# Performance work log

Hardware: AMD Instinct MI355X
Metric: run time of the kernel (lower is better)

## Reference

```python
import jax, jax.numpy as jnp
import numpy as np

DIM = 768
INNER = int(DIM * 0.125)  # 96
N_TOK = 8
EPS = 1e-5


def setup_inputs() -> dict:
    key = jax.random.key(0)
    ks = jax.random.split(key, 5)
    x = jax.random.normal(ks[0], (64, DIM, 32, 32), dtype=jnp.float32)
    gamma = jnp.ones((DIM,), jnp.float32)
    beta = jnp.zeros((DIM,), jnp.float32)
    w1 = jax.random.normal(ks[1], (DIM, INNER), jnp.float32) * 0.02
    b1 = jnp.zeros((INNER,), jnp.float32)
    w2 = jax.random.normal(ks[2], (INNER, N_TOK), jnp.float32) * 0.02
    b2 = jnp.zeros((N_TOK,), jnp.float32)
    return {"x": x, "gamma": gamma, "beta": beta, "w1": w1, "b1": b1, "w2": w2, "b2": b2}


def reference(x, gamma, beta, w1, b1, w2, b2):
    B, C, H, W = x.shape
    # torch: x.transpose(1, 3).reshape(B, H*W, C)  ([B,C,H,W] -> [B,W,H,C] -> [B,HW,C])
    t = jnp.transpose(x, (0, 3, 2, 1)).reshape(B, H * W, C)
    # LayerNorm over channel dim
    mu = jnp.mean(t, axis=-1, keepdims=True)
    var = jnp.mean(jnp.square(t - mu), axis=-1, keepdims=True)
    xn = (t - mu) * jax.lax.rsqrt(var + EPS) * gamma + beta  # [B, HW, C]
    # small MLP producing per-token attention logits
    h = jax.nn.gelu(xn @ w1 + b1, approximate=False)  # [B, HW, INNER]
    attn = jax.nn.softmax(h @ w2 + b2, axis=1)        # softmax across HW -> [B, HW, N]
    # (x.unsqueeze(-1) * attn).mean(dim=1) == einsum / HW, no [B,HW,C,N] intermediate
    out = jnp.einsum('bhc,bhn->bcn', xn, attn) / (H * W)  # [B, C, N]
    return out
```

## Files before the change

kernel.cpp:

```cpp
#include <hip/hip_runtime.h>
#include <hip/hip_bf16.h>
#include <math.h>

#define BATCH 64
#define CH    768
#define NP    1024
#define NI    96
#define NT    8
#define EPSF  1e-5f

typedef __attribute__((ext_vector_type(8))) short  short8;
typedef __attribute__((ext_vector_type(4))) float  f32x4;

__device__ __forceinline__ short bfs(float f) {
    __hip_bfloat16 h = __float2bfloat16(f);
    return *reinterpret_cast<short*>(&h);
}

__global__ __launch_bounds__(64) void k_w1pack(const float* __restrict__ w1,
                                               unsigned short* __restrict__ w1f) {
    int ks = blockIdx.x / 6, nt = blockIdx.x % 6;
    int l  = threadIdx.x;
    int n  = nt * 16 + (l & 15);
    int k0 = ks * 32 + (l >> 4) * 8;
    short8 o;
#pragma unroll
    for (int j = 0; j < 8; ++j) o[j] = bfs(w1[(size_t)(k0 + j) * NI + n]);
    *(short8*)(w1f + ((size_t)blockIdx.x * 64 + l) * 8) = o;
}

__global__ __launch_bounds__(256) void k_mlpf(const float* __restrict__ x,
        const float* __restrict__ gamma, const float* __restrict__ beta,
        const unsigned short* __restrict__ w1f,
        const float* __restrict__ b1, const float* __restrict__ w2,
        const float* __restrict__ b2,
        float2* __restrict__ stats, float* __restrict__ logits)
{
    int bid = blockIdx.x;
    int b   = bid >> 3;
    int p0  = (bid & 7) << 7;
    int tid = threadIdx.x;

    __shared__ float4 ls[8][32];
    __shared__ float4 lq[8][32];
    __shared__ float2 stl[128];

    {
        int tg = tid & 31;
        int cg = tid >> 5;
        const float* xb = x + (size_t)b * CH * NP + p0 + tg * 4;
        float4 s = make_float4(0.f,0.f,0.f,0.f);
        float4 q = make_float4(0.f,0.f,0.f,0.f);
#pragma unroll 4
        for (int c = cg; c < CH; c += 8) {
            float4 v = *(const float4*)(xb + (size_t)c * NP);
            s.x += v.x; s.y += v.y; s.z += v.z; s.w += v.w;
            q.x += v.x*v.x; q.y += v.y*v.y; q.z += v.z*v.z; q.w += v.w*v.w;
        }
        ls[cg][tg] = s; lq[cg][tg] = q;
        __syncthreads();
        if (cg == 0) {
#pragma unroll
            for (int k = 1; k < 8; ++k) {
                float4 s2 = ls[k][tg], q2 = lq[k][tg];
                s.x += s2.x; s.y += s2.y; s.z += s2.z; s.w += s2.w;
                q.x += q2.x; q.y += q2.y; q.z += q2.z; q.w += q2.w;
            }
            const float inv = 1.0f / (float)CH;
            float2 r0, r1, r2, r3;
            float mu, var;
            mu = s.x*inv; var = q.x*inv - mu*mu; r0 = make_float2(mu, rsqrtf(var + EPSF));
            mu = s.y*inv; var = q.y*inv - mu*mu; r1 = make_float2(mu, rsqrtf(var + EPSF));
            mu = s.z*inv; var = q.z*inv - mu*mu; r2 = make_float2(mu, rsqrtf(var + EPSF));
            mu = s.w*inv; var = q.w*inv - mu*mu; r3 = make_float2(mu, rsqrtf(var + EPSF));
            stl[tg*4+0] = r0; stl[tg*4+1] = r1; stl[tg*4+2] = r2; stl[tg*4+3] = r3;
            float2* st = stats + (size_t)b * NP + p0 + tg * 4;
            st[0] = r0; st[1] = r1; st[2] = r2; st[3] = r3;
        }
        __syncthreads();
    }

    int wv   = tid >> 6;
    int lane = tid & 63;
    int m    = lane & 15;
    int kg   = lane >> 4;
    int mt   = p0 + wv * 32;

    float2 st0 = stl[wv * 32 + m];
    float2 st1 = stl[wv * 32 + 16 + m];
    const float* xb = x + (size_t)b * CH * NP + mt + m;

    f32x4 accA[6], accB[6];
#pragma unroll
    for (int nt = 0; nt < 6; ++nt) {
        accA[nt] = (f32x4){0.f,0.f,0.f,0.f};
        accB[nt] = (f32x4){0.f,0.f,0.f,0.f};
    }
    const short8* wfp = (const short8*)w1f;

    for (int ks = 0; ks < 24; ++ks) {
        int cb = ks * 32 + kg * 8;
        const float* xc = xb + (size_t)cb * NP;
        float xv0[8], xv1[8];
#pragma unroll
        for (int j = 0; j < 8; ++j) {
            xv0[j] = xc[(size_t)j * NP];
            xv1[j] = xc[(size_t)j * NP + 16];
        }
        float4 g0 = *(const float4*)(gamma + cb);
        float4 g1 = *(const float4*)(gamma + cb + 4);
        float4 e0 = *(const float4*)(beta  + cb);
        float4 e1 = *(const float4*)(beta  + cb + 4);
        float gm[8] = {g0.x,g0.y,g0.z,g0.w,g1.x,g1.y,g1.z,g1.w};
        float bt[8] = {e0.x,e0.y,e0.z,e0.w,e1.x,e1.y,e1.z,e1.w};
        short8 a0, a1;
#pragma unroll
        for (int j = 0; j < 8; ++j) {
            float rg0 = st0.y * gm[j];
            float rg1 = st1.y * gm[j];
            a0[j] = bfs(fmaf(xv0[j], rg0, fmaf(-st0.x, rg0, bt[j])));
            a1[j] = bfs(fmaf(xv1[j], rg1, fmaf(-st1.x, rg1, bt[j])));
        }
        const short8* wk = wfp + (size_t)ks * 6 * 64 + lane;
#pragma unroll
        for (int nt = 0; nt < 6; ++nt) {
            short8 bf = wk[nt * 64];
            accA[nt] = __builtin_amdgcn_mfma_f32_16x16x32_bf16(a0, bf, accA[nt], 0, 0, 0);
            accB[nt] = __builtin_amdgcn_mfma_f32_16x16x32_bf16(a1, bf, accB[nt], 0, 0, 0);
        }
    }

    int nlo = lane & 15;
    float4 b2a = *(const float4*)b2;
    float4 b2b = *(const float4*)(b2 + 4);
#pragma unroll
    for (int half = 0; half < 2; ++half) {
        float lg[4][8];
#pragma unroll
        for (int r = 0; r < 4; ++r)
#pragma unroll
            for (int t = 0; t < 8; ++t) lg[r][t] = 0.f;
#pragma unroll
        for (int nt = 0; nt < 6; ++nt) {
            int n = nt * 16 + nlo;
            float b1v = b1[n];
            float4 w2a = *(const float4*)(w2 + n * 8);
            float4 w2b = *(const float4*)(w2 + n * 8 + 4);
            f32x4 ac = half ? accB[nt] : accA[nt];
#pragma unroll
            for (int r = 0; r < 4; ++r) {
                float h = ac[r] + b1v;
                h = 0.5f * h * (1.0f + erff(h * 0.70710678118654752f));
                lg[r][0] += h * w2a.x; lg[r][1] += h * w2a.y;
                lg[r][2] += h * w2a.z; lg[r][3] += h * w2a.w;
                lg[r][4] += h * w2b.x; lg[r][5] += h * w2b.y;
                lg[r][6] += h * w2b.z; lg[r][7] += h * w2b.w;
            }
        }
#pragma unroll
        for (int mask = 1; mask <= 8; mask <<= 1)
#pragma unroll
            for (int r = 0; r < 4; ++r)
#pragma unroll
                for (int t = 0; t < 8; ++t)
                    lg[r][t] += __shfl_xor(lg[r][t], mask, 64);
        if (nlo == 0) {
#pragma unroll
            for (int r = 0; r < 4; ++r) {
                int pp = mt + half * 16 + kg * 4 + r;
                float* op = logits + ((size_t)b * NP + pp) * NT;
                *(float4*)op       = make_float4(lg[r][0] + b2a.x, lg[r][1] + b2a.y,
                                                 lg[r][2] + b2a.z, lg[r][3] + b2a.w);
                *(float4*)(op + 4) = make_float4(lg[r][4] + b2b.x, lg[r][5] + b2b.y,
                                                 lg[r][6] + b2b.z, lg[r][7] + b2b.w);
            }
        }
    }
}

__global__ __launch_bounds__(256) void k_g(const float* __restrict__ logits,
        const float2* __restrict__ stats,
        unsigned short* __restrict__ gbf, float* __restrict__ S2)
{
    int b = blockIdx.x;
    int tid = threadIdx.x;
    int lane = tid & 63, wv = tid >> 6;
    __shared__ float gs[NP][NT];
    __shared__ float red[4][16];

    const float* lgp = logits + (size_t)b * NP * NT;
    const float2* stb = stats + (size_t)b * NP;
    float e[4][NT];
    float2 st4[4];
#pragma unroll
    for (int k = 0; k < 4; ++k) {
        int p = tid + 256 * k;
        float4 a  = *(const float4*)(lgp + (size_t)p * NT);
        float4 bq = *(const float4*)(lgp + (size_t)p * NT + 4);
        e[k][0]=a.x; e[k][1]=a.y; e[k][2]=a.z; e[k][3]=a.w;
        e[k][4]=bq.x; e[k][5]=bq.y; e[k][6]=bq.z; e[k][7]=bq.w;
        st4[k] = stb[p];
    }
    float mx[NT];
#pragma unroll
    for (int t = 0; t < NT; ++t)
        mx[t] = fmaxf(fmaxf(e[0][t], e[1][t]), fmaxf(e[2][t], e[3][t]));
#pragma unroll
    for (int mask = 1; mask <= 32; mask <<= 1)
#pragma unroll
        for (int t = 0; t < NT; ++t)
            mx[t] = fmaxf(mx[t], __shfl_xor(mx[t], mask, 64));
    if (lane == 0) {
#pragma unroll
        for (int t = 0; t < NT; ++t) red[wv][t] = mx[t];
    }
    __syncthreads();
#pragma unroll
    for (int t = 0; t < NT; ++t)
        mx[t] = fmaxf(fmaxf(red[0][t], red[1][t]), fmaxf(red[2][t], red[3][t]));
    __syncthreads();

    float sm[NT], s2p[NT];
#pragma unroll
    for (int t = 0; t < NT; ++t) { sm[t] = 0.f; s2p[t] = 0.f; }
#pragma unroll
    for (int k = 0; k < 4; ++k) {
        float mr = st4[k].x * st4[k].y;
#pragma unroll
        for (int t = 0; t < NT; ++t) {
            e[k][t] = expf(e[k][t] - mx[t]);
            sm[t]  += e[k][t];
            s2p[t] += mr * e[k][t];
        }
    }
#pragma unroll
    for (int mask = 1; mask <= 32; mask <<= 1)
#pragma unroll
        for (int t = 0; t < NT; ++t) {
            sm[t]  += __shfl_xor(sm[t],  mask, 64);
            s2p[t] += __shfl_xor(s2p[t], mask, 64);
        }
    if (lane == 0) {
#pragma unroll
        for (int t = 0; t < NT; ++t) { red[wv][t] = sm[t]; red[wv][8 + t] = s2p[t]; }
    }
    __syncthreads();
    float inv[NT], s2f[NT];
#pragma unroll
    for (int t = 0; t < NT; ++t) {
        float s  = red[0][t] + red[1][t] + red[2][t] + red[3][t];
        float s2 = red[0][8+t] + red[1][8+t] + red[2][8+t] + red[3][8+t];
        inv[t] = 1.0f / s;
        s2f[t] = s2 * inv[t];
    }
    if (tid < NT) S2[b * NT + tid] = s2f[tid];

#pragma unroll
    for (int k = 0; k < 4; ++k)
#pragma unroll
        for (int t = 0; t < NT; ++t)
            gs[tid + 256 * k][t] = st4[k].y * e[k][t] * inv[t];
    __syncthreads();

    unsigned short* gb = gbf + (size_t)b * 2048 * 8;
#pragma unroll
    for (int ss = 0; ss < 8; ++ss) {
        int slot   = tid * 8 + ss;
        int lane_s = slot & 63;
        int ks     = slot >> 6;
        int n      = lane_s & 15;
        int k0     = ks * 32 + (lane_s >> 4) * 8;
        short8 o = (short8){0,0,0,0,0,0,0,0};
        if (n < 8) {
#pragma unroll
            for (int j = 0; j < 8; ++j) o[j] = bfs(gs[k0 + j][n]);
        }
        *(short8*)(gb + (size_t)slot * 8) = o;
    }
}

__global__ __launch_bounds__(256) void k_outg(const float* __restrict__ x,
        const unsigned short* __restrict__ gbf, const float* __restrict__ S2,
        const float* __restrict__ gamma, const float* __restrict__ beta,
        float* __restrict__ out)
{
    int b   = blockIdx.x / 12;
    int c0  = (blockIdx.x % 12) * 64;
    int tid = threadIdx.x, lane = tid & 63, wv = tid >> 6;
    int kg  = lane >> 4, m = lane & 15, n = lane & 15;
    int cw  = c0 + wv * 16;

    const float*  xr = x + ((size_t)b * CH + cw + m) * NP + kg * 8;
    const short8* gb = (const short8*)gbf + (size_t)b * 2048;

    f32x4 acc0 = (f32x4){0.f,0.f,0.f,0.f};
    f32x4 acc1 = (f32x4){0.f,0.f,0.f,0.f};
#pragma unroll 4
    for (int ks = 0; ks < 32; ks += 2) {
        float4 v0 = *(const float4*)(xr + ks * 32);
        float4 v1 = *(const float4*)(xr + ks * 32 + 4);
        float4 v2 = *(const float4*)(xr + ks * 32 + 32);
        float4 v3 = *(const float4*)(xr + ks * 32 + 36);
        short8 a0, a1;
        a0[0]=bfs(v0.x); a0[1]=bfs(v0.y); a0[2]=bfs(v0.z); a0[3]=bfs(v0.w);
        a0[4]=bfs(v1.x); a0[5]=bfs(v1.y); a0[6]=bfs(v1.z); a0[7]=bfs(v1.w);
        a1[0]=bfs(v2.x); a1[1]=bfs(v2.y); a1[2]=bfs(v2.z); a1[3]=bfs(v2.w);
        a1[4]=bfs(v3.x); a1[5]=bfs(v3.y); a1[6]=bfs(v3.z); a1[7]=bfs(v3.w);
        short8 bf0 = gb[ks * 64 + lane];
        short8 bf1 = gb[(ks + 1) * 64 + lane];
        acc0 = __builtin_amdgcn_mfma_f32_16x16x32_bf16(a0, bf0, acc0, 0, 0, 0);
        acc1 = __builtin_amdgcn_mfma_f32_16x16x32_bf16(a1, bf1, acc1, 0, 0, 0);
    }

    if (n < NT) {
        float s2v = S2[b * NT + n];
        const float sc = 1.0f / (float)NP;
#pragma unroll
        for (int r = 0; r < 4; ++r) {
            int c = cw + kg * 4 + r;
            float val = acc0[r] + acc1[r];
            out[((size_t)b * CH + c) * NT + n] = (gamma[c] * (val - s2v) + beta[c]) * sc;
        }
    }
}

extern "C" void kernel_launch(void* const* d_in, const int* in_sizes, int n_in,
                              void* d_out, int out_size, void* d_ws, size_t ws_size,
                              hipStream_t stream) {
    const float* x     = (const float*)d_in[0];
    const float* gamma = (const float*)d_in[1];
    const float* beta  = (const float*)d_in[2];
    const float* w1    = (const float*)d_in[3];
    const float* b1    = (const float*)d_in[4];
    const float* w2    = (const float*)d_in[5];
    const float* b2    = (const float*)d_in[6];
    float* out = (float*)d_out;

    char* ws = (char*)d_ws;
    float2*         stats = (float2*)(ws + 0);
    float*          lgbuf = (float*)(ws + 524288);
    unsigned short* w1f   = (unsigned short*)(ws + 2621440);
    unsigned short* gbf   = (unsigned short*)(ws + 2768896);
    float*          S2    = (float*)(ws + 4866048);

    k_w1pack<<<24 * 6,     64,  0, stream>>>(w1, w1f);
    k_mlpf  <<<BATCH * 8,  256, 0, stream>>>(x, gamma, beta, w1f, b1, w2, b2, stats, lgbuf);
    k_g     <<<BATCH,      256, 0, stream>>>(lgbuf, stats, gbf, S2);
    k_outg  <<<BATCH * 12, 256, 0, stream>>>(x, gbf, S2, gamma, beta, out);
}
```

Measured before the change: 353.8 us.

## Fold LayerNorm into W1 GEMM epilogue and fuse softmax weights into output kernel

Gamma is folded into packed W1, and the per-column sums gamma·W1 and beta·W1+b1 are precomputed. This lets the MLP kernel feed raw x into the MFMA and apply mean/rstd afterwards, so the separate statistics pass over x is gone. The softmax/g-fragment kernel is merged into the output kernel, which recomputes the per-batch softmax in each block and keeps the bf16 fragments in LDS instead of a global round trip. The costs are redundant softmax work across 12 blocks per batch, larger LDS use, and bf16 rounding of un-normalized x, which may lose precision when the mean is large.

```diff
diff --git a/kernel.cpp b/kernel.cpp
--- a/kernel.cpp
+++ b/kernel.cpp
@@ -17,77 +17,55 @@
     return *reinterpret_cast<short*>(&h);
 }
 
-__global__ __launch_bounds__(64) void k_w1pack(const float* __restrict__ w1,
-                                               unsigned short* __restrict__ w1f) {
-    int ks = blockIdx.x / 6, nt = blockIdx.x % 6;
-    int l  = threadIdx.x;
-    int n  = nt * 16 + (l & 15);
-    int k0 = ks * 32 + (l >> 4) * 8;
-    short8 o;
-#pragma unroll
-    for (int j = 0; j < 8; ++j) o[j] = bfs(w1[(size_t)(k0 + j) * NI + n]);
-    *(short8*)(w1f + ((size_t)blockIdx.x * 64 + l) * 8) = o;
+__global__ __launch_bounds__(128) void k_prep(const float* __restrict__ w1,
+        const float* __restrict__ gamma, const float* __restrict__ beta,
+        const float* __restrict__ b1,
+        unsigned short* __restrict__ w1f, float* __restrict__ c1, float* __restrict__ gw1)
+{
+    int bid = blockIdx.x;
+    if (bid < 72) {
+        int slot = bid * 128 + threadIdx.x;
+        int l    = slot & 63;
+        int blk  = slot >> 6;
+        int ks   = blk / 6, nt = blk % 6;
+        int n    = nt * 16 + (l & 15);
+        int k0   = ks * 32 + (l >> 4) * 8;
+        short8 o;
+#pragma unroll
+        for (int j = 0; j < 8; ++j)
+            o[j] = bfs(gamma[k0 + j] * w1[(size_t)(k0 + j) * NI + n]);
+        *(short8*)(w1f + (size_t)slot * 8) = o;
+    } else {
+        int n = threadIdx.x;
+        if (n < NI) {
+            float bw = 0.f, gw = 0.f;
+#pragma unroll 4
+            for (int c = 0; c < CH; ++c) {
+                float w = w1[(size_t)c * NI + n];
+                bw = fmaf(beta[c],  w, bw);
+                gw = fmaf(gamma[c], w, gw);
+            }
+            c1[n]  = bw + b1[n];
+            gw1[n] = gw;
+        }
+    }
 }
 
 __global__ __launch_bounds__(256) void k_mlpf(const float* __restrict__ x,
-        const float* __restrict__ gamma, const float* __restrict__ beta,
         const unsigned short* __restrict__ w1f,
-        const float* __restrict__ b1, const float* __restrict__ w2,
-        const float* __restrict__ b2,
+        const float* __restrict__ c1, const float* __restrict__ gw1,
+        const float* __restrict__ w2, const float* __restrict__ b2,
         float2* __restrict__ stats, float* __restrict__ logits)
 {
-    int bid = blockIdx.x;
-    int b   = bid >> 3;
-    int p0  = (bid & 7) << 7;
-    int tid = threadIdx.x;
-
-    __shared__ float4 ls[8][32];
-    __shared__ float4 lq[8][32];
-    __shared__ float2 stl[128];
-
-    {
-        int tg = tid & 31;
-        int cg = tid >> 5;
-        const float* xb = x + (size_t)b * CH * NP + p0 + tg * 4;
-        float4 s = make_float4(0.f,0.f,0.f,0.f);
-        float4 q = make_float4(0.f,0.f,0.f,0.f);
-#pragma unroll 4
-        for (int c = cg; c < CH; c += 8) {
-            float4 v = *(const float4*)(xb + (size_t)c * NP);
-            s.x += v.x; s.y += v.y; s.z += v.z; s.w += v.w;
-            q.x += v.x*v.x; q.y += v.y*v.y; q.z += v.z*v.z; q.w += v.w*v.w;
-        }
-        ls[cg][tg] = s; lq[cg][tg] = q;
-        __syncthreads();
-        if (cg == 0) {
-#pragma unroll
-            for (int k = 1; k < 8; ++k) {
-                float4 s2 = ls[k][tg], q2 = lq[k][tg];
-                s.x += s2.x; s.y += s2.y; s.z += s2.z; s.w += s2.w;
-                q.x += q2.x; q.y += q2.y; q.z += q2.z; q.w += q2.w;
-            }
-            const float inv = 1.0f / (float)CH;
-            float2 r0, r1, r2, r3;
-            float mu, var;
-            mu = s.x*inv; var = q.x*inv - mu*mu; r0 = make_float2(mu, rsqrtf(var + EPSF));
-            mu = s.y*inv; var = q.y*inv - mu*mu; r1 = make_float2(mu, rsqrtf(var + EPSF));
-            mu = s.z*inv; var = q.z*inv - mu*mu; r2 = make_float2(mu, rsqrtf(var + EPSF));
-            mu = s.w*inv; var = q.w*inv - mu*mu; r3 = make_float2(mu, rsqrtf(var + EPSF));
-            stl[tg*4+0] = r0; stl[tg*4+1] = r1; stl[tg*4+2] = r2; stl[tg*4+3] = r3;
-            float2* st = stats + (size_t)b * NP + p0 + tg * 4;
-            st[0] = r0; st[1] = r1; st[2] = r2; st[3] = r3;
-        }
-        __syncthreads();
-    }
-
-    int wv   = tid >> 6;
-    int lane = tid & 63;
+    int bid  = blockIdx.x;
+    int b    = bid >> 3;
+    int p0   = (bid & 7) << 7;
+    int wv   = threadIdx.x >> 6;
+    int lane = threadIdx.x & 63;
     int m    = lane & 15;
     int kg   = lane >> 4;
     int mt   = p0 + wv * 32;
 
-    float2 st0 = stl[wv * 32 + m];
-    float2 st1 = stl[wv * 32 + 16 + m];
     const float* xb = x + (size_t)b * CH * NP + mt + m;
 
     f32x4 accA[6], accB[6];
@@ -96,6 +74,7 @@
         accA[nt] = (f32x4){0.f,0.f,0.f,0.f};
         accB[nt] = (f32x4){0.f,0.f,0.f,0.f};
     }
+    float s0 = 0.f, q0 = 0.f, s1 = 0.f, q1 = 0.f;
     const short8* wfp = (const short8*)w1f;
 
     for (int ks = 0; ks < 24; ++ks) {
@@ -107,19 +86,13 @@
             xv0[j] = xc[(size_t)j * NP];
             xv1[j] = xc[(size_t)j * NP + 16];
         }
-        float4 g0 = *(const float4*)(gamma + cb);
-        float4 g1 = *(const float4*)(gamma + cb + 4);
-        float4 e0 = *(const float4*)(beta  + cb);
-        float4 e1 = *(const float4*)(beta  + cb + 4);
-        float gm[8] = {g0.x,g0.y,g0.z,g0.w,g1.x,g1.y,g1.z,g1.w};
-        float bt[8] = {e0.x,e0.y,e0.z,e0.w,e1.x,e1.y,e1.z,e1.w};
         short8 a0, a1;
 #pragma unroll
         for (int j = 0; j < 8; ++j) {
-            float rg0 = st0.y * gm[j];
-            float rg1 = st1.y * gm[j];
-            a0[j] = bfs(fmaf(xv0[j], rg0, fmaf(-st0.x, rg0, bt[j])));
-            a1[j] = bfs(fmaf(xv1[j], rg1, fmaf(-st1.x, rg1, bt[j])));
+            s0 += xv0[j]; q0 = fmaf(xv0[j], xv0[j], q0);
+            s1 += xv1[j]; q1 = fmaf(xv1[j], xv1[j], q1);
+            a0[j] = bfs(xv0[j]);
+            a1[j] = bfs(xv1[j]);
         }
         const short8* wk = wfp + (size_t)ks * 6 * 64 + lane;
 #pragma unroll
@@ -130,6 +103,32 @@
         }
     }
 
+    s0 += __shfl_xor(s0, 16, 64); s0 += __shfl_xor(s0, 32, 64);
+    q0 += __shfl_xor(q0, 16, 64); q0 += __shfl_xor(q0, 32, 64);
+    s1 += __shfl_xor(s1, 16, 64); s1 += __shfl_xor(s1, 32, 64);
+    q1 += __shfl_xor(q1, 16, 64); q1 += __shfl_xor(q1, 32, 64);
+    const float invC = 1.0f / (float)CH;
+    float mu0 = s0 * invC, var0 = fmaf(-mu0, mu0, q0 * invC);
+    float mu1 = s1 * invC, var1 = fmaf(-mu1, mu1, q1 * invC);
+    float rstd0 = rsqrtf(var0 + EPSF), rstd1 = rsqrtf(var1 + EPSF);
+    float mr0 = mu0 * rstd0, mr1 = mu1 * rstd1;
+
+    if (kg == 0) {
+        float2* st = stats + (size_t)b * NP + mt + m;
+        st[0]  = make_float2(mr0, rstd0);
+        st[16] = make_float2(mr1, rstd1);
+    }
+
+    float mrs0[4], rss0[4], mrs1[4], rss1[4];
+#pragma unroll
+    for (int r = 0; r < 4; ++r) {
+        int src = 4 * kg + r;
+        mrs0[r] = __shfl(mr0,   src, 64);
+        rss0[r] = __shfl(rstd0, src, 64);
+        mrs1[r] = __shfl(mr1,   src, 64);
+        rss1[r] = __shfl(rstd1, src, 64);
+    }
+
     int nlo = lane & 15;
     float4 b2a = *(const float4*)b2;
     float4 b2b = *(const float4*)(b2 + 4);
@@ -143,13 +142,16 @@
 #pragma unroll
         for (int nt = 0; nt < 6; ++nt) {
             int n = nt * 16 + nlo;
-            float b1v = b1[n];
+            float c1v  = c1[n];
+            float gw1v = gw1[n];
             float4 w2a = *(const float4*)(w2 + n * 8);
             float4 w2b = *(const float4*)(w2 + n * 8 + 4);
             f32x4 ac = half ? accB[nt] : accA[nt];
 #pragma unroll
             for (int r = 0; r < 4; ++r) {
-                float h = ac[r] + b1v;
+                float rs = half ? rss1[r] : rss0[r];
+                float mr = half ? mrs1[r] : mrs0[r];
+                float h = fmaf(rs, ac[r], fmaf(-mr, gw1v, c1v));
                 h = 0.5f * h * (1.0f + erff(h * 0.70710678118654752f));
                 lg[r][0] += h * w2a.x; lg[r][1] += h * w2a.y;
                 lg[r][2] += h * w2a.z; lg[r][3] += h * w2a.w;
@@ -178,15 +180,19 @@
     }
 }
 
-__global__ __launch_bounds__(256) void k_g(const float* __restrict__ logits,
-        const float2* __restrict__ stats,
-        unsigned short* __restrict__ gbf, float* __restrict__ S2)
+__global__ __launch_bounds__(256) void k_outg(const float* __restrict__ x,
+        const float* __restrict__ logits, const float2* __restrict__ stats,
+        const float* __restrict__ gamma, const float* __restrict__ beta,
+        float* __restrict__ out)
 {
-    int b = blockIdx.x;
+    int b   = blockIdx.x / 12;
+    int c0  = (blockIdx.x % 12) * 64;
     int tid = threadIdx.x;
     int lane = tid & 63, wv = tid >> 6;
-    __shared__ float gs[NP][NT];
+
+    __shared__ unsigned short gfrag[2048 * 8];
     __shared__ float red[4][16];
+    __shared__ float s2s[NT];
 
     const float* lgp = logits + (size_t)b * NP * NT;
     const float2* stb = stats + (size_t)b * NP;
@@ -225,12 +231,11 @@
     for (int t = 0; t < NT; ++t) { sm[t] = 0.f; s2p[t] = 0.f; }
 #pragma unroll
     for (int k = 0; k < 4; ++k) {
-        float mr = st4[k].x * st4[k].y;
 #pragma unroll
         for (int t = 0; t < NT; ++t) {
             e[k][t] = expf(e[k][t] - mx[t]);
             sm[t]  += e[k][t];
-            s2p[t] += mr * e[k][t];
+            s2p[t] = fmaf(st4[k].x, e[k][t], s2p[t]);
         }
     }
 #pragma unroll
@@ -242,56 +247,43 @@
         }
     if (lane == 0) {
 #pragma unroll
-        for (int t = 0; t < NT; ++t) { red[wv][t] = sm[t]; red[wv][8 + t] = s2p[t]; }
-    }
-    __syncthreads();
-    float inv[NT], s2f[NT];
-#pragma unroll
-    for (int t = 0; t < NT; ++t) {
-        float s  = red[0][t] + red[1][t] + red[2][t] + red[3][t];
-        float s2 = red[0][8+t] + red[1][8+t] + red[2][8+t] + red[3][8+t];
-        inv[t] = 1.0f / s;
-        s2f[t] = s2 * inv[t];
-    }
-    if (tid < NT) S2[b * NT + tid] = s2f[tid];
-
-#pragma unroll
-    for (int k = 0; k < 4; ++k)
+        for (int t = 0; t < NT; ++t) { red[wv][t] = sm[t]; }
+    }
+    __syncthreads();
+    float inv[NT];
+#pragma unroll
+    for (int t = 0; t < NT; ++t)
+        inv[t] = 1.0f / (red[0][t] + red[1][t] + red[2][t] + red[3][t]);
+    __syncthreads();
+    if (lane == 0) {
+#pragma unroll
+        for (int t = 0; t < NT; ++t) red[wv][t] = s2p[t];
+    }
+    __syncthreads();
+    if (tid < NT)
+        s2s[tid] = (red[0][tid] + red[1][tid] + red[2][tid] + red[3][tid]) * inv[tid];
+
+#pragma unroll
+    for (int q = 0; q < 4; ++q) {
+        int idx  = tid * 4 + q;
+        int slot = (idx >> 3) * 16 + 8 + (idx & 7);
+        *(short8*)(gfrag + (size_t)slot * 8) = (short8){0,0,0,0,0,0,0,0};
+    }
+#pragma unroll
+    for (int k = 0; k < 4; ++k) {
+        int p = tid + 256 * k;
+        int base = ((p >> 5) * 64 + ((p >> 3) & 3) * 16) * 8 + (p & 7);
+        float rs = st4[k].y;
 #pragma unroll
         for (int t = 0; t < NT; ++t)
-            gs[tid + 256 * k][t] = st4[k].y * e[k][t] * inv[t];
-    __syncthreads();
-
-    unsigned short* gb = gbf + (size_t)b * 2048 * 8;
-#pragma unroll
-    for (int ss = 0; ss < 8; ++ss) {
-        int slot   = tid * 8 + ss;
-        int lane_s = slot & 63;
-        int ks     = slot >> 6;
-        int n      = lane_s & 15;
-        int k0     = ks * 32 + (lane_s >> 4) * 8;
-        short8 o = (short8){0,0,0,0,0,0,0,0};
-        if (n < 8) {
-#pragma unroll
-            for (int j = 0; j < 8; ++j) o[j] = bfs(gs[k0 + j][n]);
-        }
-        *(short8*)(gb + (size_t)slot * 8) = o;
-    }
-}
-
-__global__ __launch_bounds__(256) void k_outg(const float* __restrict__ x,
-        const unsigned short* __restrict__ gbf, const float* __restrict__ S2,
-        const float* __restrict__ gamma, const float* __restrict__ beta,
-        float* __restrict__ out)
-{
-    int b   = blockIdx.x / 12;
-    int c0  = (blockIdx.x % 12) * 64;
-    int tid = threadIdx.x, lane = tid & 63, wv = tid >> 6;
-    int kg  = lane >> 4, m = lane & 15, n = lane & 15;
-    int cw  = c0 + wv * 16;
-
+            gfrag[base + t * 8] = (unsigned short)bfs(rs * e[k][t] * inv[t]);
+    }
+    __syncthreads();
+
+    int kg = lane >> 4, m = lane & 15, n = lane & 15;
+    int cw = c0 + wv * 16;
     const float*  xr = x + ((size_t)b * CH + cw + m) * NP + kg * 8;
-    const short8* gb = (const short8*)gbf + (size_t)b * 2048;
+    const short8* gb = (const short8*)gfrag;
 
     f32x4 acc0 = (f32x4){0.f,0.f,0.f,0.f};
     f32x4 acc1 = (f32x4){0.f,0.f,0.f,0.f};
@@ -313,7 +305,7 @@
     }
 
     if (n < NT) {
-        float s2v = S2[b * NT + n];
+        float s2v = s2s[n];
         const float sc = 1.0f / (float)NP;
 #pragma unroll
         for (int r = 0; r < 4; ++r) {
@@ -340,11 +332,10 @@
     float2*         stats = (float2*)(ws + 0);
     float*          lgbuf = (float*)(ws + 524288);
     unsigned short* w1f   = (unsigned short*)(ws + 2621440);
-    unsigned short* gbf   = (unsigned short*)(ws + 2768896);
-    float*          S2    = (float*)(ws + 4866048);
-
-    k_w1pack<<<24 * 6,     64,  0, stream>>>(w1, w1f);
-    k_mlpf  <<<BATCH * 8,  256, 0, stream>>>(x, gamma, beta, w1f, b1, w2, b2, stats, lgbuf);
-    k_g     <<<BATCH,      256, 0, stream>>>(lgbuf, stats, gbf, S2);
-    k_outg  <<<BATCH * 12, 256, 0, stream>>>(x, gbf, S2, gamma, beta, out);
-}
+    float*          c1    = (float*)(ws + 2768896);
+    float*          gw1   = (float*)(ws + 2769280);
+
+    k_prep<<<73,         128, 0, stream>>>(w1, gamma, beta, b1, w1f, c1, gw1);
+    k_mlpf<<<BATCH * 8,  256, 0, stream>>>(x, w1f, c1, gw1, w2, b2, stats, lgbuf);
+    k_outg<<<BATCH * 12, 256, 0, stream>>>(x, lgbuf, stats, gamma, beta, out);
+}
```

Result: slower. 386.8 us (+9.3%).
